# Optimization experiments

Measured on AMD Instinct MI355X. Metric: run time of the kernel, lower is better.

## Reference

```python
import jax, jax.numpy as jnp
import numpy as np

# yolov5 non_max_suppression defaults (from forward's input_parameters.get defaults)
CONF_THRES = 0.25
IOU_THRES = 0.45
MAX_DET = 1000        # max detections returned per image
TOP_K = 4096          # fixed candidate count entering greedy NMS (jit-friendly stand-in for max_nms)
MAX_WH = 7680.0       # per-class box offset so NMS is class-aware (yolov5 trick)


def setup_inputs() -> dict:
    key = jax.random.key(0)
    k1, k2, k3, k4 = jax.random.split(key, 4)
    B, N, NC = 16, 25200, 80  # 640x640 yolov5 -> 25200 anchors, 80 COCO classes
    xy = jax.random.uniform(k1, (B, N, 2)) * 640.0            # box centers in pixels
    wh = jax.random.uniform(k2, (B, N, 2)) * 160.0 + 4.0       # box sizes
    obj = jax.random.uniform(k3, (B, N, 1))                    # objectness
    cls = jax.random.uniform(k4, (B, N, NC))                   # class scores
    pred = jnp.concatenate([xy, wh, obj, cls], axis=-1)        # [B, N, 85]
    return {"pred": pred}


def _xywh2xyxy(x):
    xy, wh = x[..., :2], x[..., 2:4]
    return jnp.concatenate([xy - wh * 0.5, xy + wh * 0.5], axis=-1)


def _iou_one_vs_all(box, boxes):
    # box [4], boxes [K,4], xyxy
    lt = jnp.maximum(box[:2], boxes[:, :2])
    rb = jnp.minimum(box[2:], boxes[:, 2:])
    wh = jnp.clip(rb - lt, 0.0)
    inter = wh[:, 0] * wh[:, 1]
    a1 = (box[2] - box[0]) * (box[3] - box[1])
    a2 = (boxes[:, 2] - boxes[:, 0]) * (boxes[:, 3] - boxes[:, 1])
    return inter / (a1 + a2 - inter + 1e-7)


def _nms_single(pred):
    # pred [N, 5+nc] raw yolov5 output for one image
    obj = pred[:, 4:5]
    scores_all = pred[:, 5:] * obj                 # conf = obj_conf * cls_conf
    conf = scores_all.max(axis=-1)                 # best-class confidence [N]
    cls = scores_all.argmax(axis=-1).astype(pred.dtype)
    boxes = _xywh2xyxy(pred[:, :4])                # [N,4] xyxy

    valid = conf > CONF_THRES
    s = jnp.where(valid, conf, -1.0)
    order = jnp.argsort(-s)[:TOP_K]                # top candidates by score
    b = boxes[order]                               # [K,4]
    sc = s[order]                                  # [K]
    c = cls[order]                                 # [K]
    ob = b + c[:, None] * MAX_WH                   # class-offset boxes for class-aware NMS

    ar = jnp.arange(TOP_K)

    def step(supp, i):
        alive = (~supp[i]) & (sc[i] > 0.0)
        iou = _iou_one_vs_all(ob[i], ob)
        supp = supp | (alive & (iou > IOU_THRES) & (ar > i))
        return supp, alive

    _, keep = jax.lax.scan(step, jnp.zeros(TOP_K, dtype=bool), ar)

    fs = jnp.where(keep, sc, -1.0)
    idx = jnp.argsort(-fs)[:MAX_DET]               # kept boxes, score-sorted
    det = jnp.concatenate([b[idx], fs[idx][:, None], c[idx][:, None]], axis=-1)  # [max_det,6]
    ok = fs[idx] > 0.0
    return jnp.where(ok[:, None], det, 0.0)        # zero-padded [max_det, 6] (x1,y1,x2,y2,conf,cls)


def reference(pred):
    # [B, max_det, 6] padded detections per image
    return jax.vmap(_nms_single)(pred)
```

## Files before the change

### kernel.cpp

```cpp
#include <hip/hip_runtime.h>

#define BATCH  16
#define NPRED  25200
#define NCLS   80
#define CDIM   85
#define TOPK   4096
#define NBUCK  4096
#define MAXDET 1000
#define CONF_T 0.25f
#define IOU_T  0.45f
#define MAXWH  7680.0f
#define ORD_BASE 0xBE800000u

typedef unsigned long long u64;
typedef unsigned int u32;
typedef unsigned short u16;
typedef unsigned char u8;

__device__ __forceinline__ u64 umax64(u64 a, u64 b) { return a > b ? a : b; }
__device__ __forceinline__ u64 umin64(u64 a, u64 b) { return a < b ? a : b; }

__device__ __forceinline__ void cx_u64(u64* a, int i, int p, bool desc) {
    u64 x = a[i], y = a[p];
    if (desc ? (x < y) : (x > y)) { a[i] = y; a[p] = x; }
}


__device__ void hybrid_sort4096_desc_ks(u64 r[4], u64* a, int kstart) {
    const int tid = threadIdx.x;
    for (int k = kstart; k <= 4096; k <<= 1) {
        if (k >= 512) {
            int jmax = (k >> 1) > 2048 ? 2048 : (k >> 1);
#pragma unroll
            for (int e = 0; e < 4; ++e) a[4 * tid + e] = r[e];
            __syncthreads();
            for (int j = jmax; j >= 256; j >>= 1) {
#pragma unroll
                for (int t2 = 0; t2 < 2; ++t2) {
                    int q = (t2 << 10) | tid;
                    int i = ((q & ~(j - 1)) << 1) | (q & (j - 1));
                    cx_u64(a, i, i | j, (i & k) == 0);
                }
                __syncthreads();
            }
#pragma unroll
            for (int e = 0; e < 4; ++e) r[e] = a[4 * tid + e];
            __syncthreads();
        }
        {
            int jstart = (k >> 1) > 128 ? 128 : (k >> 1);
            bool desc = (((4 * tid) & k) == 0);
            for (int j = jstart; j >= 4; j >>= 1) {
                int m = j >> 2;
                bool take_max = (((tid & m) == 0) == desc);
#pragma unroll
                for (int e = 0; e < 4; ++e) {
                    u64 v = __shfl_xor(r[e], m, 64);
                    r[e] = take_max ? umax64(r[e], v) : umin64(r[e], v);
                }
            }
        }
        if (k >= 4) {
            bool desc = (((4 * tid) & k) == 0);
            u64 x0 = r[0], x2 = r[2];
            r[0] = desc ? umax64(x0, x2) : umin64(x0, x2);
            r[2] = desc ? umin64(x0, x2) : umax64(x0, x2);
            u64 x1 = r[1], x3 = r[3];
            r[1] = desc ? umax64(x1, x3) : umin64(x1, x3);
            r[3] = desc ? umin64(x1, x3) : umax64(x1, x3);
        }
        {
            bool d01 = (((4 * tid + 0) & k) == 0);
            bool d23 = (((4 * tid + 2) & k) == 0);
            u64 x0 = r[0], x1 = r[1];
            r[0] = d01 ? umax64(x0, x1) : umin64(x0, x1);
            r[1] = d01 ? umin64(x0, x1) : umax64(x0, x1);
            u64 x2 = r[2], x3 = r[3];
            r[2] = d23 ? umax64(x2, x3) : umin64(x2, x3);
            r[3] = d23 ? umin64(x2, x3) : umax64(x2, x3);
        }
    }
}


__device__ void hybrid_sort1024_dir(u64 r[4], u64* a, bool fdesc) {
    const int tid = threadIdx.x;
    for (int k = 2; k <= 1024; k <<= 1) {
        if (k >= 512) {
            int jmax = (k >> 1) > 512 ? 512 : (k >> 1);
#pragma unroll
            for (int e = 0; e < 4; ++e) a[4 * tid + e] = r[e];
            __syncthreads();
            for (int j = jmax; j >= 256; j >>= 1) {
#pragma unroll
                for (int t2 = 0; t2 < 2; ++t2) {
                    int q = (t2 << 8) | tid;
                    int i = ((q & ~(j - 1)) << 1) | (q & (j - 1));
                    cx_u64(a, i, i | j, ((i & k) == 0) == fdesc);
                }
                __syncthreads();
            }
#pragma unroll
            for (int e = 0; e < 4; ++e) r[e] = a[4 * tid + e];
            __syncthreads();
        }
        {
            int jstart = (k >> 1) > 128 ? 128 : (k >> 1);
            bool desc = ((((4 * tid) & k) == 0) == fdesc);
            for (int j = jstart; j >= 4; j >>= 1) {
                int m = j >> 2;
                bool take_max = (((tid & m) == 0) == desc);
#pragma unroll
                for (int e = 0; e < 4; ++e) {
                    u64 v = __shfl_xor(r[e], m, 64);
                    r[e] = take_max ? umax64(r[e], v) : umin64(r[e], v);
                }
            }
        }
        if (k >= 4) {
            bool desc = ((((4 * tid) & k) == 0) == fdesc);
            u64 x0 = r[0], x2 = r[2];
            r[0] = desc ? umax64(x0, x2) : umin64(x0, x2);
            r[2] = desc ? umin64(x0, x2) : umax64(x0, x2);
            u64 x1 = r[1], x3 = r[3];
            r[1] = desc ? umax64(x1, x3) : umin64(x1, x3);
            r[3] = desc ? umin64(x1, x3) : umax64(x1, x3);
        }
        {
            bool d01 = ((((4 * tid + 0) & k) == 0) == fdesc);
            bool d23 = ((((4 * tid + 2) & k) == 0) == fdesc);
            u64 x0 = r[0], x1 = r[1];
            r[0] = d01 ? umax64(x0, x1) : umin64(x0, x1);
            r[1] = d01 ? umin64(x0, x1) : umax64(x0, x1);
            u64 x2 = r[2], x3 = r[3];
            r[2] = d23 ? umax64(x2, x3) : umin64(x2, x3);
            r[3] = d23 ? umin64(x2, x3) : umax64(x2, x3);
        }
    }
}

__device__ void wave_sort256_desc(u64 r[4]) {
    const int lane = threadIdx.x & 63;
    for (int k = 2; k <= 256; k <<= 1) {
        int jstart = (k >> 1) > 128 ? 128 : (k >> 1);
        bool desc = (((4 * lane) & k) == 0);
        for (int j = jstart; j >= 4; j >>= 1) {
            int m = j >> 2;
            bool take_max = (((lane & m) == 0) == desc);
#pragma unroll
            for (int e = 0; e < 4; ++e) {
                u64 v = __shfl_xor(r[e], m, 64);
                r[e] = take_max ? umax64(r[e], v) : umin64(r[e], v);
            }
        }
        if (k >= 4) {
            u64 x0 = r[0], x2 = r[2];
            r[0] = desc ? umax64(x0, x2) : umin64(x0, x2);
            r[2] = desc ? umin64(x0, x2) : umax64(x0, x2);
            u64 x1 = r[1], x3 = r[3];
            r[1] = desc ? umax64(x1, x3) : umin64(x1, x3);
            r[3] = desc ? umin64(x1, x3) : umax64(x1, x3);
        }
        {
            bool d01 = (((4 * lane + 0) & k) == 0);
            bool d23 = (((4 * lane + 2) & k) == 0);
            u64 x0 = r[0], x1 = r[1];
            r[0] = d01 ? umax64(x0, x1) : umin64(x0, x1);
            r[1] = d01 ? umin64(x0, x1) : umax64(x0, x1);
            u64 x2 = r[2], x3 = r[3];
            r[2] = d23 ? umax64(x2, x3) : umin64(x2, x3);
            r[3] = d23 ? umin64(x2, x3) : umax64(x2, x3);
        }
    }
}


__global__ __launch_bounds__(256) void k1_score(const float* __restrict__ pred,
                                                u64* __restrict__ keys) {
    const int lane = threadIdx.x & 63;
    const int l16 = lane & 15;
    const long long gw = (long long)blockIdx.x * 4 + (threadIdx.x >> 6);
    const long long rowIdx = gw * 4 + (lane >> 4);
    const int b = (int)(rowIdx / NPRED);
    const int n = (int)(rowIdx - (long long)b * NPRED);
    const float* row = pred + rowIdx * CDIM;
    float obj = row[4];
    u64 m = 0ull;
#pragma unroll
    for (int k = 0; k < 5; ++k) {
        int c = l16 + 16 * k;
        float v = row[5 + c] * obj;
        u64 mk = ((u64)(__float_as_uint(v) | 0x80000000u) << 32) | (u64)(u32)(NCLS - 1 - c);
        if (mk > m) m = mk;
    }
#pragma unroll
    for (int o = 8; o > 0; o >>= 1) {
        u64 other = __shfl_xor(m, o, 64);
        if (other > m) m = other;
    }
    if (l16 == 0) {
        float best = __uint_as_float((u32)(m >> 32) & 0x7FFFFFFFu);
        int cls = (NCLS - 1) - (int)(m & 0x7Fu);
        float s = (best > CONF_T) ? best : -1.0f;
        u32 u = __float_as_uint(s);
        u32 ord = (u & 0x80000000u) ? ~u : (u | 0x80000000u);
        keys[rowIdx] = ((u64)ord << 32) | ((u64)(u32)(32767 - n) << 7) | (u64)(u32)cls;
    }
}


__global__ __launch_bounds__(1024) void k2a(const u64* __restrict__ keys,
                                            u64* __restrict__ topUn,
                                            u8* __restrict__ keep) {
    __shared__ u64 smem[4096];
    __shared__ u64 side[1024];
    __shared__ u32 hist[4096];
    __shared__ u32 wsum[16];
    __shared__ int sh_T, sh_C1, sh_R, c1pos, sidepos;
    const int b = blockIdx.x;
    const int tid = threadIdx.x;
    const int lane = tid & 63;
    const int wid = tid >> 6;
    const u64 lanelt = (1ull << lane) - 1ull;

#pragma unroll
    for (int e = 0; e < 4; ++e) { smem[4 * tid + e] = 0ull; hist[4 * tid + e] = 0u; }
    side[tid] = 0ull;
    ((u32*)keep)[b * 1024 + tid] = 0u;
    __syncthreads();

    const u64* kb = keys + (long long)b * NPRED;
    for (int it = 0; it < (NPRED + 1023) / 1024; ++it) {
        int n = it * 1024 + tid;
        if (n < NPRED) {
            u32 hi = (u32)(kb[n] >> 32);
            if (hi > ORD_BASE) atomicAdd(&hist[(hi - ORD_BASE - 1u) >> 12], 1u);
        }
    }
    __syncthreads();

    u32 h[4];
    u32 tsum = 0;
#pragma unroll
    for (int e = 0; e < 4; ++e) {
        h[e] = hist[NBUCK - 1 - (4 * tid + e)];
        tsum += h[e];
    }
    u32 inc = tsum;
    for (int o = 1; o < 64; o <<= 1) {
        u32 v = __shfl_up(inc, o, 64);
        if (lane >= o) inc += v;
    }
    if (lane == 63) wsum[wid] = inc;
    __syncthreads();
    if (tid == 0) {
        u32 run = 0;
        for (int i = 0; i < 16; ++i) { u32 t = wsum[i]; wsum[i] = run; run += t; }
        sh_T = -1; sh_C1 = (int)run; sh_R = 0;
        c1pos = 0; sidepos = 0;
    }
    __syncthreads();
    {
        u32 cum = wsum[wid] + (inc - tsum);
#pragma unroll
        for (int e = 0; e < 4; ++e) {
            if (h[e] > 0 && cum < (u32)TOPK && cum + h[e] >= (u32)TOPK) {
                sh_T = NBUCK - 1 - (4 * tid + e);
                sh_C1 = (int)cum;
                sh_R = TOPK - (int)cum;
            }
            cum += h[e];
        }
    }
    __syncthreads();
    const int T = sh_T, C1 = sh_C1, R = sh_R;

    for (int it = 0; it < (NPRED + 1023) / 1024; ++it) {
        int n = it * 1024 + tid;
        bool act = n < NPRED;
        u64 key = act ? kb[n] : 0ull;
        u32 hi = (u32)(key >> 32);
        bool v = act && (hi > ORD_BASE);
        int bt = v ? (int)((hi - ORD_BASE - 1u) >> 12) : -1;
        bool t1 = v && (bt > T);
        bool t2 = v && (bt == T);
        u64 m1 = __ballot(t1), m2 = __ballot(t2);
        int b1 = 0, b2 = 0;
        if (lane == 0) {
            if (m1) b1 = atomicAdd(&c1pos, (int)__popcll(m1));
            if (m2) b2 = atomicAdd(&sidepos, (int)__popcll(m2));
        }
        b1 = __shfl(b1, 0, 64);
        b2 = __shfl(b2, 0, 64);
        if (t1) smem[b1 + __popcll(m1 & lanelt)] = key;
        if (t2) { int s2 = b2 + __popcll(m2 & lanelt); if (s2 < 1024) side[s2] = key; }
    }
    __syncthreads();

    if (R > 0) {
        int cntT = sidepos;
        if (cntT <= 256) {
            if (wid == 0) {
                u64 r[4];
#pragma unroll
                for (int e = 0; e < 4; ++e) r[e] = side[4 * lane + e];
                wave_sort256_desc(r);
#pragma unroll
                for (int e = 0; e < 4; ++e) side[4 * lane + e] = r[e];
            }
        } else {
            for (int k = 2; k <= 1024; k <<= 1) {
                for (int j = k >> 1; j >= 1; j >>= 1) {
                    if (tid < 512) {
                        int q = tid;
                        int i = ((q & ~(j - 1)) << 1) | (q & (j - 1));
                        cx_u64(side, i, i | j, (i & k) == 0);
                    }
                    __syncthreads();
                }
            }
        }
        __syncthreads();
        if (tid < R) smem[C1 + tid] = side[tid];
    }
    __syncthreads();

    for (int i = tid; i < 4096; i += 1024) topUn[(long long)b * TOPK + i] = smem[i];
}


__global__ __launch_bounds__(256) void k2b(u64* __restrict__ topUn) {
    __shared__ u64 a[1024];
    const int tid = threadIdx.x;
    const int s = blockIdx.x & 3;
    const long long base = (long long)blockIdx.x * 1024;
    u64 r[4];
#pragma unroll
    for (int e = 0; e < 4; ++e) r[e] = topUn[base + 4 * tid + e];
    hybrid_sort1024_dir(r, a, (s & 1) == 0);
#pragma unroll
    for (int e = 0; e < 4; ++e) topUn[base + 4 * tid + e] = r[e];
}


__global__ __launch_bounds__(1024) void k2c(const u64* __restrict__ topUn,
                                            u64* __restrict__ topSorted) {
    __shared__ u64 a[4096];
    const int b = blockIdx.x;
    const int tid = threadIdx.x;
    u64 r[4];
#pragma unroll
    for (int e = 0; e < 4; ++e) r[e] = topUn[(long long)b * TOPK + 4 * tid + e];
    hybrid_sort4096_desc_ks(r, a, 2048);
#pragma unroll
    for (int e = 0; e < 4; ++e) topSorted[(long long)b * TOPK + 4 * tid + e] = r[e];
}


__global__ __launch_bounds__(64) void k3_nms(const float* __restrict__ pred,
                                             const u64* __restrict__ topSorted,
                                             u8* __restrict__ keep) {
    const int b = blockIdx.x;
    const int c = blockIdx.y;
    const int lane = threadIdx.x;
    __shared__ u32 list[4096];
    __shared__ float4 sbox[1024];
    __shared__ u8 suppb[4096];
    const u64* tb = topSorted + (long long)b * TOPK;
    const u64 lanelt = (1ull << lane) - 1ull;

    u32 pos = 0;
    for (int it = 0; it < 64; ++it) {
        u64 key = tb[it * 64 + lane];
        u32 hi = (u32)(key >> 32);
        bool mine = (hi > 0x80000000u) && ((int)(key & 0x7Fu) == c);
        u64 m = __ballot(mine);
        if (mine)
            list[pos + __popcll(m & lanelt)] =
                ((u32)(it * 64 + lane) << 15) | (32767u - (u32)((key >> 7) & 0x7FFFu));
        pos += (u32)__popcll(m);
    }
    const int n = (int)pos;
    if (n == 0) return;
    u8* kb = keep + b * TOPK;
    const float off = (float)c * MAXWH;

    if (n <= 128) {
        u32 r0 = 0, r1 = 0;
        float4 b0 = make_float4(0.0f, 0.0f, 0.0f, 0.0f);
        float4 b1 = make_float4(0.0f, 0.0f, 0.0f, 0.0f);
        if (lane < n) {
            u32 e = list[lane];
            r0 = e >> 15;
            const float* row = pred + ((long long)b * NPRED + (int)(e & 0x7FFFu)) * CDIM;
            float x = row[0], y = row[1], w = row[2], hh = row[3];
            b0.x = (x - w * 0.5f) + off;
            b0.y = (y - hh * 0.5f) + off;
            b0.z = (x + w * 0.5f) + off;
            b0.w = (y + hh * 0.5f) + off;
        }
        if (64 + lane < n) {
            u32 e = list[64 + lane];
            r1 = e >> 15;
            const float* row = pred + ((long long)b * NPRED + (int)(e & 0x7FFFu)) * CDIM;
            float x = row[0], y = row[1], w = row[2], hh = row[3];
            b1.x = (x - w * 0.5f) + off;
            b1.y = (y - hh * 0.5f) + off;
            b1.z = (x + w * 0.5f) + off;
            b1.w = (y + hh * 0.5f) + off;
        }
        {
#pragma clang fp contract(off)
            float a20 = (b0.z - b0.x) * (b0.w - b0.y);
            float a21 = (b1.z - b1.x) * (b1.w - b1.y);
            u64 rem0 = (n >= 64) ? ~0ull : ((1ull << n) - 1ull);
            u64 rem1 = (n > 64) ? ((n >= 128) ? ~0ull : ((1ull << (n - 64)) - 1ull)) : 0ull;
            u64 keep0 = 0ull, keep1 = 0ull;
            const bool two = (n > 64);
            while (rem0) {
                int ii = __builtin_ctzll(rem0);
                rem0 &= ~(1ull << ii);
                keep0 |= 1ull << ii;
                float bix = __shfl(b0.x, ii, 64);
                float biy = __shfl(b0.y, ii, 64);
                float biz = __shfl(b0.z, ii, 64);
                float biw = __shfl(b0.w, ii, 64);
                float a1  = __shfl(a20, ii, 64);
                {
                    float ltx = fmaxf(bix, b0.x), lty = fmaxf(biy, b0.y);
                    float rbx = fminf(biz, b0.z), rby = fminf(biw, b0.w);
                    float ww = fmaxf(rbx - ltx, 0.0f), hh = fmaxf(rby - lty, 0.0f);
                    float inter = ww * hh;
                    float iou = inter / (((a1 + a20) - inter) + 1e-7f);
                    bool k0 = (iou > IOU_T) && (lane > ii);
                    rem0 &= ~__ballot(k0);
                }
                if (two) {
                    float ltx = fmaxf(bix, b1.x), lty = fmaxf(biy, b1.y);
                    float rbx = fminf(biz, b1.z), rby = fminf(biw, b1.w);
                    float ww = fmaxf(rbx - ltx, 0.0f), hh = fmaxf(rby - lty, 0.0f);
                    float inter = ww * hh;
                    float iou = inter / (((a1 + a21) - inter) + 1e-7f);
                    bool k1 = (iou > IOU_T);
                    rem1 &= ~__ballot(k1);
                }
            }
            while (rem1) {
                int ii = __builtin_ctzll(rem1);
                rem1 &= ~(1ull << ii);
                keep1 |= 1ull << ii;
                float bix = __shfl(b1.x, ii, 64);
                float biy = __shfl(b1.y, ii, 64);
                float biz = __shfl(b1.z, ii, 64);
                float biw = __shfl(b1.w, ii, 64);
                float a1  = __shfl(a21, ii, 64);
                float ltx = fmaxf(bix, b1.x), lty = fmaxf(biy, b1.y);
                float rbx = fminf(biz, b1.z), rby = fminf(biw, b1.w);
                float ww = fmaxf(rbx - ltx, 0.0f), hh = fmaxf(rby - lty, 0.0f);
                float inter = ww * hh;
                float iou = inter / (((a1 + a21) - inter) + 1e-7f);
                bool k1 = (iou > IOU_T) && (lane > ii);
                rem1 &= ~__ballot(k1);
            }
            if ((keep0 >> lane) & 1ull) kb[r0] = 1;
            if ((keep1 >> lane) & 1ull) kb[r1] = 1;
        }
    } else {
        for (int j = lane; j < 1024; j += 64) {
            if (j < n) {
                u32 e = list[j];
                const float* row = pred + ((long long)b * NPRED + (int)(e & 0x7FFFu)) * CDIM;
                float x = row[0], y = row[1], w = row[2], hh = row[3];
                float4 o;
                o.x = (x - w * 0.5f) + off;
                o.y = (y - hh * 0.5f) + off;
                o.z = (x + w * 0.5f) + off;
                o.w = (y + hh * 0.5f) + off;
                sbox[j] = o;
            }
        }
        for (int j = lane; j < n; j += 64) suppb[j] = 0;
        __syncthreads();
        volatile u8* supp = suppb;
        {
#pragma clang fp contract(off)
            for (int ii = 0; ii < n; ++ii) {
                if (supp[ii]) continue;
                u32 ei = list[ii];
                int ri = (int)(ei >> 15);
                if (lane == 0) kb[ri] = 1;
                float4 bi;
                if (ii < 1024) bi = sbox[ii];
                else {
                    const float* row = pred + ((long long)b * NPRED + (int)(ei & 0x7FFFu)) * CDIM;
                    float x = row[0], y = row[1], w = row[2], hh = row[3];
                    bi.x = (x - w * 0.5f) + off;
                    bi.y = (y - hh * 0.5f) + off;
                    bi.z = (x + w * 0.5f) + off;
                    bi.w = (y + hh * 0.5f) + off;
                }
                float a1 = (bi.z - bi.x) * (bi.w - bi.y);
                for (int jj = ii + 1 + lane; jj < n; jj += 64) {
                    float4 bj;
                    if (jj < 1024) bj = sbox[jj];
                    else {
                        u32 ej = list[jj];
                        const float* row = pred + ((long long)b * NPRED + (int)(ej & 0x7FFFu)) * CDIM;
                        float x = row[0], y = row[1], w = row[2], hh = row[3];
                        bj.x = (x - w * 0.5f) + off;
                        bj.y = (y - hh * 0.5f) + off;
                        bj.z = (x + w * 0.5f) + off;
                        bj.w = (y + hh * 0.5f) + off;
                    }
                    float ltx = fmaxf(bi.x, bj.x), lty = fmaxf(bi.y, bj.y);
                    float rbx = fminf(bi.z, bj.z), rby = fminf(bi.w, bj.w);
                    float ww = fmaxf(rbx - ltx, 0.0f), hh = fmaxf(rby - lty, 0.0f);
                    float inter = ww * hh;
                    float a2 = (bj.z - bj.x) * (bj.w - bj.y);
                    float iou = inter / (((a1 + a2) - inter) + 1e-7f);
                    if (iou > IOU_T) supp[jj] = 1;
                }
                __syncthreads();
            }
        }
    }
}


__global__ __launch_bounds__(256) void k4_out(const float* __restrict__ pred,
                                              const u64* __restrict__ topSorted,
                                              const u8* __restrict__ keep,
                                              float* __restrict__ out) {
    const int b = blockIdx.x;
    const int tid = threadIdx.x;
    __shared__ u64 words[64];
    __shared__ int wpre[64];
    float* outb = out + (long long)b * MAXDET * 6;
    for (int i = tid; i < MAXDET * 6; i += 256) outb[i] = 0.0f;
    const u8* kp = keep + b * 4096;
    if (tid < 64) {
        u64 w = 0ull;
        const u64* k8 = (const u64*)(kp + tid * 64);
#pragma unroll
        for (int q = 0; q < 8; ++q) {
            u64 v = k8[q];
#pragma unroll
            for (int bb = 0; bb < 8; ++bb)
                if ((v >> (8 * bb)) & 0xFFull) w |= 1ull << (q * 8 + bb);
        }
        words[tid] = w;
    }
    __syncthreads();
    if (tid == 0) {
        int run = 0;
        for (int t = 0; t < 64; ++t) { wpre[t] = run; run += __popcll(words[t]); }
    }
    __syncthreads();
    const u64* kb = topSorted + (long long)b * TOPK;
    for (int r = tid; r < 4096; r += 256) {
        int wd = r >> 6;
        if ((words[wd] >> (r & 63)) & 1ull) {
            int pos = wpre[wd] + __popcll(words[wd] & ((1ull << (r & 63)) - 1ull));
            if (pos < MAXDET) {
                u64 key = kb[r];
                u32 hi = (u32)(key >> 32);
                int n = 32767 - (int)((key >> 7) & 0x7FFFu);
                const float* row = pred + ((long long)b * NPRED + n) * CDIM;
                float x = row[0], y = row[1], w2 = row[2], h = row[3];
                float* o = outb + pos * 6;
                o[0] = x - w2 * 0.5f;
                o[1] = y - h * 0.5f;
                o[2] = x + w2 * 0.5f;
                o[3] = y + h * 0.5f;
                o[4] = __uint_as_float(hi & 0x7FFFFFFFu);
                o[5] = (float)(key & 0x7Fu);
            }
        }
    }
}


extern "C" void kernel_launch(void* const* d_in, const int* in_sizes, int n_in,
                              void* d_out, int out_size, void* d_ws, size_t ws_size,
                              hipStream_t stream) {
    const float* pred = (const float*)d_in[0];
    float* out = (float*)d_out;

    char* ws = (char*)d_ws;
    u64* keys      = (u64*)ws;
    u64* topUn     = (u64*)(ws + 3225600);
    u64* topSorted = (u64*)(ws + 3749888);
    u8*  keep      = (u8*)(ws + 4274176);

    hipLaunchKernelGGL(k1_score, dim3(BATCH * NPRED / 16), dim3(256), 0, stream,
                       pred, keys);
    hipLaunchKernelGGL(k2a, dim3(BATCH), dim3(1024), 0, stream, keys, topUn, keep);
    hipLaunchKernelGGL(k2b, dim3(BATCH * 4), dim3(256), 0, stream, topUn);
    hipLaunchKernelGGL(k2c, dim3(BATCH), dim3(1024), 0, stream, topUn, topSorted);
    hipLaunchKernelGGL(k3_nms, dim3(BATCH, NCLS), dim3(64), 0, stream,
                       pred, topSorted, keep);
    hipLaunchKernelGGL(k4_out, dim3(BATCH), dim3(256), 0, stream, pred, topSorted, keep, out);
}
```

Before: 286.0 us.

## Fuse top-K sort into selection kernel and output into NMS via last-block counter

Folds the separate 1024-chunk sort and 4096 merge kernels into the selection kernel, sorting directly in shared memory instead of round-tripping through a global buffer. It also removes the output kernel: each per-class NMS block increments an atomic counter per image, and the last block to finish compacts the keep flags and writes the detections. This cuts three kernel launches and their global memory traffic. In exchange, the sort now runs on only 16 blocks, and a single 64-thread wave does the output compaction.

```diff
diff --git a/kernel.cpp b/kernel.cpp
--- a/kernel.cpp
+++ b/kernel.cpp
@@ -83,33 +83,32 @@
 }
 
 
-__device__ void hybrid_sort1024_dir(u64 r[4], u64* a, bool fdesc) {
-    const int tid = threadIdx.x;
+__device__ void group_sort1024_dir(u64 r[4], u64* a, int gtid, bool fdesc) {
     for (int k = 2; k <= 1024; k <<= 1) {
         if (k >= 512) {
             int jmax = (k >> 1) > 512 ? 512 : (k >> 1);
 #pragma unroll
-            for (int e = 0; e < 4; ++e) a[4 * tid + e] = r[e];
+            for (int e = 0; e < 4; ++e) a[4 * gtid + e] = r[e];
             __syncthreads();
             for (int j = jmax; j >= 256; j >>= 1) {
 #pragma unroll
                 for (int t2 = 0; t2 < 2; ++t2) {
-                    int q = (t2 << 8) | tid;
+                    int q = (t2 << 8) | gtid;
                     int i = ((q & ~(j - 1)) << 1) | (q & (j - 1));
                     cx_u64(a, i, i | j, ((i & k) == 0) == fdesc);
                 }
                 __syncthreads();
             }
 #pragma unroll
-            for (int e = 0; e < 4; ++e) r[e] = a[4 * tid + e];
+            for (int e = 0; e < 4; ++e) r[e] = a[4 * gtid + e];
             __syncthreads();
         }
         {
             int jstart = (k >> 1) > 128 ? 128 : (k >> 1);
-            bool desc = ((((4 * tid) & k) == 0) == fdesc);
+            bool desc = ((((4 * gtid) & k) == 0) == fdesc);
             for (int j = jstart; j >= 4; j >>= 1) {
                 int m = j >> 2;
-                bool take_max = (((tid & m) == 0) == desc);
+                bool take_max = (((gtid & m) == 0) == desc);
 #pragma unroll
                 for (int e = 0; e < 4; ++e) {
                     u64 v = __shfl_xor(r[e], m, 64);
@@ -118,7 +117,7 @@
             }
         }
         if (k >= 4) {
-            bool desc = ((((4 * tid) & k) == 0) == fdesc);
+            bool desc = ((((4 * gtid) & k) == 0) == fdesc);
             u64 x0 = r[0], x2 = r[2];
             r[0] = desc ? umax64(x0, x2) : umin64(x0, x2);
             r[2] = desc ? umin64(x0, x2) : umax64(x0, x2);
@@ -127,8 +126,8 @@
             r[3] = desc ? umin64(x1, x3) : umax64(x1, x3);
         }
         {
-            bool d01 = ((((4 * tid + 0) & k) == 0) == fdesc);
-            bool d23 = ((((4 * tid + 2) & k) == 0) == fdesc);
+            bool d01 = ((((4 * gtid + 0) & k) == 0) == fdesc);
+            bool d23 = ((((4 * gtid + 2) & k) == 0) == fdesc);
             u64 x0 = r[0], x1 = r[1];
             r[0] = d01 ? umax64(x0, x1) : umin64(x0, x1);
             r[1] = d01 ? umin64(x0, x1) : umax64(x0, x1);
@@ -209,9 +208,10 @@
 }
 
 
-__global__ __launch_bounds__(1024) void k2a(const u64* __restrict__ keys,
-                                            u64* __restrict__ topUn,
-                                            u8* __restrict__ keep) {
+__global__ __launch_bounds__(1024) void k2_sel(const u64* __restrict__ keys,
+                                               u64* __restrict__ topSorted,
+                                               u8* __restrict__ keep,
+                                               u32* __restrict__ done) {
     __shared__ u64 smem[4096];
     __shared__ u64 side[1024];
     __shared__ u32 hist[4096];
@@ -227,6 +227,7 @@
     for (int e = 0; e < 4; ++e) { smem[4 * tid + e] = 0ull; hist[4 * tid + e] = 0u; }
     side[tid] = 0ull;
     ((u32*)keep)[b * 1024 + tid] = 0u;
+    if (tid == 0) done[b] = 0u;
     __syncthreads();
 
     const u64* kb = keys + (long long)b * NPRED;
@@ -325,47 +326,34 @@
     }
     __syncthreads();
 
-    for (int i = tid; i < 4096; i += 1024) topUn[(long long)b * TOPK + i] = smem[i];
-}
-
-
-__global__ __launch_bounds__(256) void k2b(u64* __restrict__ topUn) {
-    __shared__ u64 a[1024];
-    const int tid = threadIdx.x;
-    const int s = blockIdx.x & 3;
-    const long long base = (long long)blockIdx.x * 1024;
-    u64 r[4];
-#pragma unroll
-    for (int e = 0; e < 4; ++e) r[e] = topUn[base + 4 * tid + e];
-    hybrid_sort1024_dir(r, a, (s & 1) == 0);
-#pragma unroll
-    for (int e = 0; e < 4; ++e) topUn[base + 4 * tid + e] = r[e];
-}
-
-
-__global__ __launch_bounds__(1024) void k2c(const u64* __restrict__ topUn,
-                                            u64* __restrict__ topSorted) {
-    __shared__ u64 a[4096];
-    const int b = blockIdx.x;
-    const int tid = threadIdx.x;
-    u64 r[4];
-#pragma unroll
-    for (int e = 0; e < 4; ++e) r[e] = topUn[(long long)b * TOPK + 4 * tid + e];
-    hybrid_sort4096_desc_ks(r, a, 2048);
-#pragma unroll
-    for (int e = 0; e < 4; ++e) topSorted[(long long)b * TOPK + 4 * tid + e] = r[e];
+    {
+        const int g = tid >> 8;
+        const int gtid = tid & 255;
+        u64* ga = smem + (g << 10);
+        u64 r[4];
+#pragma unroll
+        for (int e = 0; e < 4; ++e) r[e] = ga[4 * gtid + e];
+        group_sort1024_dir(r, ga, gtid, (g & 1) == 0);
+        hybrid_sort4096_desc_ks(r, smem, 2048);
+#pragma unroll
+        for (int e = 0; e < 4; ++e) topSorted[(long long)b * TOPK + 4 * tid + e] = r[e];
+    }
 }
 
 
 __global__ __launch_bounds__(64) void k3_nms(const float* __restrict__ pred,
                                              const u64* __restrict__ topSorted,
-                                             u8* __restrict__ keep) {
+                                             u8* __restrict__ keep,
+                                             u32* __restrict__ done,
+                                             float* __restrict__ out) {
     const int b = blockIdx.x;
     const int c = blockIdx.y;
     const int lane = threadIdx.x;
     __shared__ u32 list[4096];
     __shared__ float4 sbox[1024];
     __shared__ u8 suppb[4096];
+    __shared__ u64 words[64];
+    __shared__ int wpre[64];
     const u64* tb = topSorted + (long long)b * TOPK;
     const u64 lanelt = (1ull << lane) - 1ull;
 
@@ -381,11 +369,10 @@
         pos += (u32)__popcll(m);
     }
     const int n = (int)pos;
-    if (n == 0) return;
     u8* kb = keep + b * TOPK;
     const float off = (float)c * MAXWH;
 
-    if (n <= 128) {
+    if (n > 0 && n <= 128) {
         u32 r0 = 0, r1 = 0;
         float4 b0 = make_float4(0.0f, 0.0f, 0.0f, 0.0f);
         float4 b1 = make_float4(0.0f, 0.0f, 0.0f, 0.0f);
@@ -465,7 +452,7 @@
             if ((keep0 >> lane) & 1ull) kb[r0] = 1;
             if ((keep1 >> lane) & 1ull) kb[r1] = 1;
         }
-    } else {
+    } else if (n > 128) {
         for (int j = lane; j < 1024; j += 64) {
             if (j < n) {
                 u32 e = list[j];
@@ -524,56 +511,54 @@
             }
         }
     }
-}
-
-
-__global__ __launch_bounds__(256) void k4_out(const float* __restrict__ pred,
-                                              const u64* __restrict__ topSorted,
-                                              const u8* __restrict__ keep,
-                                              float* __restrict__ out) {
-    const int b = blockIdx.x;
-    const int tid = threadIdx.x;
-    __shared__ u64 words[64];
-    __shared__ int wpre[64];
-    float* outb = out + (long long)b * MAXDET * 6;
-    for (int i = tid; i < MAXDET * 6; i += 256) outb[i] = 0.0f;
-    const u8* kp = keep + b * 4096;
-    if (tid < 64) {
-        u64 w = 0ull;
-        const u64* k8 = (const u64*)(kp + tid * 64);
-#pragma unroll
-        for (int q = 0; q < 8; ++q) {
-            u64 v = k8[q];
-#pragma unroll
-            for (int bb = 0; bb < 8; ++bb)
-                if ((v >> (8 * bb)) & 0xFFull) w |= 1ull << (q * 8 + bb);
-        }
-        words[tid] = w;
-    }
-    __syncthreads();
-    if (tid == 0) {
-        int run = 0;
-        for (int t = 0; t < 64; ++t) { wpre[t] = run; run += __popcll(words[t]); }
-    }
-    __syncthreads();
-    const u64* kb = topSorted + (long long)b * TOPK;
-    for (int r = tid; r < 4096; r += 256) {
-        int wd = r >> 6;
-        if ((words[wd] >> (r & 63)) & 1ull) {
-            int pos = wpre[wd] + __popcll(words[wd] & ((1ull << (r & 63)) - 1ull));
-            if (pos < MAXDET) {
-                u64 key = kb[r];
-                u32 hi = (u32)(key >> 32);
-                int n = 32767 - (int)((key >> 7) & 0x7FFFu);
-                const float* row = pred + ((long long)b * NPRED + n) * CDIM;
-                float x = row[0], y = row[1], w2 = row[2], h = row[3];
-                float* o = outb + pos * 6;
-                o[0] = x - w2 * 0.5f;
-                o[1] = y - h * 0.5f;
-                o[2] = x + w2 * 0.5f;
-                o[3] = y + h * 0.5f;
-                o[4] = __uint_as_float(hi & 0x7FFFFFFFu);
-                o[5] = (float)(key & 0x7Fu);
+
+    __threadfence();
+    u32 prev = 0;
+    if (lane == 0) prev = atomicAdd(&done[b], 1u);
+    prev = __shfl(prev, 0, 64);
+    if (prev == NCLS - 1) {
+        __threadfence();
+        float* outb = out + (long long)b * MAXDET * 6;
+        float4 z4 = make_float4(0.0f, 0.0f, 0.0f, 0.0f);
+        float4* ob4 = (float4*)outb;
+        for (int i = lane; i < (MAXDET * 6) / 4; i += 64) ob4[i] = z4;
+        {
+            u64 w = 0ull;
+            const u64* k8 = (const u64*)(kb + lane * 64);
+#pragma unroll
+            for (int q = 0; q < 8; ++q) {
+                u64 v = k8[q];
+#pragma unroll
+                for (int bb = 0; bb < 8; ++bb)
+                    if ((v >> (8 * bb)) & 0xFFull) w |= 1ull << (q * 8 + bb);
+            }
+            words[lane] = w;
+        }
+        __syncthreads();
+        if (lane == 0) {
+            int run = 0;
+            for (int t = 0; t < 64; ++t) { wpre[t] = run; run += __popcll(words[t]); }
+        }
+        __syncthreads();
+        for (int r = lane; r < TOPK; r += 64) {
+            int wd = r >> 6;
+            u64 wv = words[wd];
+            if ((wv >> (r & 63)) & 1ull) {
+                int p = wpre[wd] + __popcll(wv & ((1ull << (r & 63)) - 1ull));
+                if (p < MAXDET) {
+                    u64 key = tb[r];
+                    u32 hi = (u32)(key >> 32);
+                    int nn = 32767 - (int)((key >> 7) & 0x7FFFu);
+                    const float* row = pred + ((long long)b * NPRED + nn) * CDIM;
+                    float x = row[0], y = row[1], w2 = row[2], hh = row[3];
+                    float* o = outb + p * 6;
+                    o[0] = x - w2 * 0.5f;
+                    o[1] = y - hh * 0.5f;
+                    o[2] = x + w2 * 0.5f;
+                    o[3] = y + hh * 0.5f;
+                    o[4] = __uint_as_float(hi & 0x7FFFFFFFu);
+                    o[5] = (float)(key & 0x7Fu);
+                }
             }
         }
     }
@@ -588,16 +573,14 @@
 
     char* ws = (char*)d_ws;
     u64* keys      = (u64*)ws;
-    u64* topUn     = (u64*)(ws + 3225600);
-    u64* topSorted = (u64*)(ws + 3749888);
-    u8*  keep      = (u8*)(ws + 4274176);
+    u64* topSorted = (u64*)(ws + 3225600);
+    u8*  keep      = (u8*)(ws + 3749888);
+    u32* done      = (u32*)(ws + 3815424);
 
     hipLaunchKernelGGL(k1_score, dim3(BATCH * NPRED / 16), dim3(256), 0, stream,
                        pred, keys);
-    hipLaunchKernelGGL(k2a, dim3(BATCH), dim3(1024), 0, stream, keys, topUn, keep);
-    hipLaunchKernelGGL(k2b, dim3(BATCH * 4), dim3(256), 0, stream, topUn);
-    hipLaunchKernelGGL(k2c, dim3(BATCH), dim3(1024), 0, stream, topUn, topSorted);
+    hipLaunchKernelGGL(k2_sel, dim3(BATCH), dim3(1024), 0, stream,
+                       keys, topSorted, keep, done);
     hipLaunchKernelGGL(k3_nms, dim3(BATCH, NCLS), dim3(64), 0, stream,
-                       pred, topSorted, keep);
-    hipLaunchKernelGGL(k4_out, dim3(BATCH), dim3(256), 0, stream, pred, topSorted, keep, out);
-}
+                       pred, topSorted, keep, done, out);
+}
```

Result: slower. 329.8 us (+15.3%).
